# Optimization experiments

Measured on AMD Instinct MI355X. Metric: run time of the kernel, lower is better.

Reference implementation:

```python
import jax, jax.numpy as jnp
import numpy as np

B, R, S, T, D, DK = 256, 196, 200, 50, 512, 100


def setup_inputs() -> dict:
    key = jax.random.key(0)
    ks = jax.random.split(key, 20)
    inp = {
        'ifeature': jax.random.normal(ks[0], (B, R, D), jnp.float32),
        'tfeature_h': jax.random.normal(ks[1], (B, S, D), jnp.float32),
        'gfeature': jax.random.normal(ks[2], (B, S, D), jnp.float32),
        'efeature': jax.random.normal(ks[3], (B, T, D), jnp.float32),
    }
    # learned params (keras 'random_normal' init ~ stddev 0.05, 'zeros' for biases)
    lens = [R, S, S, T]
    for i in range(4):
        inp[f'w_vi{i}'] = 0.05 * jax.random.normal(ks[4 + 4 * i], (D, DK), jnp.float32)
        inp[f'w_vt{i}'] = 0.05 * jax.random.normal(ks[5 + 4 * i], (D, DK), jnp.float32)
        inp[f'w_p{i}'] = 0.05 * jax.random.normal(ks[6 + 4 * i], (2 * DK, 1), jnp.float32)
        inp[f'b{i}'] = jnp.zeros((lens[i],), jnp.float32)
    return inp


def _attend(feats, w_feat, vec, w_vec, w_p, b, vec_first):
    # feats: [B,N,D], vec: [B,D]. Score = concat(tanh parts) @ w_p + b.
    # concat+dense == split w_p into the two halves and add the partial scores.
    k = w_feat.shape[1]
    sf = jnp.tanh(jnp.einsum('bnd,dk->bnk', feats, w_feat))  # [B,N,k]
    sv = jnp.tanh(vec @ w_vec)                               # [B,k]
    if vec_first:
        wv, wf = w_p[:k, 0], w_p[k:, 0]
    else:
        wf, wv = w_p[:k, 0], w_p[k:, 0]
    score = sf @ wf + (sv @ wv)[:, None] + b                 # [B,N]
    p = jax.nn.softmax(score, axis=-1)
    return jnp.einsum('bn,bnd->bd', p, feats)                # [B,D]


def reference(ifeature, tfeature_h, gfeature, efeature,
              w_vi0, w_vt0, w_p0, b0,
              w_vi1, w_vt1, w_p1, b1,
              w_vi2, w_vt2, w_p2, b2,
              w_vi3, w_vt3, w_p3, b3):
    tfeature = jnp.mean(tfeature_h, axis=1)                  # [B,D]
    # block 0: attend over image regions, concat order (image, text)
    Vi = _attend(ifeature, w_vi0, tfeature, w_vt0, w_p0, b0, vec_first=False)
    # block 1: attend over text tokens, concat order (Vi, text)
    Vt = _attend(tfeature_h, w_vt1, Vi, w_vi1, w_p1, b1, vec_first=True)
    # block 2: attend over group feature with query Vi+Vt
    Vg = _attend(gfeature, w_vt2, Vi + Vt, w_vi2, w_p2, b2, vec_first=True)
    # block 3: attend over title feature with query Vi+Vt
    Ve = _attend(efeature, w_vt3, Vi + Vt, w_vi3, w_p3, b3, vec_first=True)
    return Vi + Vt + 0.5 * Vg + 0.5 * Ve
```

## Files before the change

kernel.cpp:

```cpp
#include <hip/hip_runtime.h>

#define DD 512
#define DKk 100
#define NT 7
#define CHUNK 16
#define MAXN 208
#define LDS_STRIDE 520

typedef __attribute__((ext_vector_type(8))) short short8;
typedef __attribute__((ext_vector_type(4))) short short4v;
typedef __attribute__((ext_vector_type(4))) float f32x4;

struct AttendArgs {
  const float* feats[4];
  const float* wfeat[4];
  const float* wf[4];
  const float* bias[4];
  int   N[4];
  float coef[4];
};

__device__ __forceinline__ short f2bf(float x) {
  unsigned u = __builtin_bit_cast(unsigned, x);
  unsigned r = (u + 0x7fffu + ((u >> 16) & 1u)) >> 16;
  return (short)r;
}

__device__ __forceinline__ float fast_tanh(float x) {
  const float e = __expf(2.0f * x);
  return 1.0f - 2.0f / (e + 1.0f);
}

__global__ void wprep_kernel(AttendArgs args, unsigned short* __restrict__ wfrag) {
  const int a = blockIdx.x / NT;
  const int t = blockIdx.x % NT;
  const int tid = threadIdx.x;
  const int lane = tid & 63;
  const int m = lane & 15;
  const int q = lane >> 4;
  const int kg = tid >> 6;
  const int col = t * 16 + m;
  const float* __restrict__ w = args.wfeat[a];
  unsigned short* __restrict__ dst = wfrag + (size_t)((a * NT + t) * 16) * 512;
  #pragma unroll
  for (int i = 0; i < 4; ++i) {
    const int ks = kg * 4 + i;
    short8 v;
    #pragma unroll
    for (int j = 0; j < 8; ++j) {
      const int d = ks * 32 + q * 8 + j;
      v[j] = (col < DKk) ? f2bf(w[d * DKk + col]) : (short)0;
    }
    *reinterpret_cast<short8*>(dst + (size_t)ks * 512 + lane * 8) = v;
  }
}

__global__ __launch_bounds__(512, 2)
void fused_kernel(AttendArgs args, const unsigned short* __restrict__ wfrag,
                  float* __restrict__ out) {
  const int a = blockIdx.x & 3;
  const int b = blockIdx.x >> 2;
  const int tid = threadIdx.x;
  const int lane = tid & 63;
  const int wave = tid >> 6;
  const int m = lane & 15;
  const int q = lane >> 4;
  const int N = args.N[a];
  const float* __restrict__ feats = args.feats[a] + (size_t)b * (size_t)N * DD;
  const float* __restrict__ wfp = args.wf[a];
  const float* __restrict__ bias = args.bias[a];

  __shared__ __align__(16) unsigned short f_lds[2][CHUNK][LDS_STRIDE];
  __shared__ float sc_part[8][MAXN];
  __shared__ float red[512];
  __shared__ float p_lds[MAXN];

  short8 bfrag[16];
  float wfv = 0.f;
  if (wave < NT) {
    const int col = wave * 16 + m;
    wfv = (col < DKk) ? wfp[col] : 0.f;
    const unsigned short* src = wfrag + (size_t)((a * NT + wave) * 16) * 512 + lane * 8;
    #pragma unroll
    for (int ks = 0; ks < 16; ++ks)
      bfrag[ks] = *reinterpret_cast<const short8*>(src + (size_t)ks * 512);
  } else {
    #pragma unroll
    for (int ks = 0; ks < 16; ++ks) bfrag[ks] = short8(0);
  }

  const int nchunks = (N + CHUNK - 1) / CHUNK;

  float4 pf[4];
  #pragma unroll
  for (int it = 0; it < 4; ++it) {
    const int idx = tid + it * 512;
    const int row = idx >> 7;
    const int c4 = idx & 127;
    pf[it] = (row < N)
      ? *reinterpret_cast<const float4*>(feats + (size_t)row * DD + (c4 << 2))
      : make_float4(0.f, 0.f, 0.f, 0.f);
  }

  for (int c = 0; c < nchunks; ++c) {
    const int bufc = c & 1;
    #pragma unroll
    for (int it = 0; it < 4; ++it) {
      const int idx = tid + it * 512;
      const int row = idx >> 7;
      const int c4 = idx & 127;
      short4v pk = { f2bf(pf[it].x), f2bf(pf[it].y), f2bf(pf[it].z), f2bf(pf[it].w) };
      *reinterpret_cast<short4v*>(&f_lds[bufc][row][c4 << 2]) = pk;
    }
    if (c + 1 < nchunks) {
      const int n0n = (c + 1) * CHUNK;
      #pragma unroll
      for (int it = 0; it < 4; ++it) {
        const int idx = tid + it * 512;
        const int row = n0n + (idx >> 7);
        const int c4 = idx & 127;
        pf[it] = (row < N)
          ? *reinterpret_cast<const float4*>(feats + (size_t)row * DD + (c4 << 2))
          : make_float4(0.f, 0.f, 0.f, 0.f);
      }
    }
    __syncthreads();

    if (wave < NT) {
      f32x4 acc = {0.f, 0.f, 0.f, 0.f};
      #pragma unroll
      for (int ks = 0; ks < 16; ++ks) {
        const short8 af = *reinterpret_cast<const short8*>(&f_lds[bufc][m][ks * 32 + q * 8]);
        acc = __builtin_amdgcn_mfma_f32_16x16x32_bf16(af, bfrag[ks], acc, 0, 0, 0);
      }
      float part[4];
      #pragma unroll
      for (int r = 0; r < 4; ++r) part[r] = fast_tanh(acc[r]) * wfv;
      #pragma unroll
      for (int mask = 1; mask <= 8; mask <<= 1) {
        #pragma unroll
        for (int r = 0; r < 4; ++r) part[r] += __shfl_xor(part[r], mask, 64);
      }
      if (m == 0) {
        #pragma unroll
        for (int r = 0; r < 4; ++r) sc_part[wave][c * 16 + q * 4 + r] = part[r];
      }
    } else if (m == 0) {
      #pragma unroll
      for (int r = 0; r < 4; ++r) sc_part[7][c * 16 + q * 4 + r] = 0.f;
    }
  }
  __syncthreads();

  float sval = -1e30f;
  if (tid < N) {
    sval = sc_part[0][tid] + sc_part[1][tid] + sc_part[2][tid] + sc_part[3][tid]
         + sc_part[4][tid] + sc_part[5][tid] + sc_part[6][tid] + sc_part[7][tid]
         + bias[tid];
  }
  red[tid] = sval;
  __syncthreads();
  for (int s = 256; s > 0; s >>= 1) {
    if (tid < s) red[tid] = fmaxf(red[tid], red[tid + s]);
    __syncthreads();
  }
  const float mx = red[0];
  __syncthreads();
  const float e = (tid < N) ? __expf(sval - mx) : 0.f;
  if (tid < MAXN) p_lds[tid] = e;
  red[tid] = e;
  __syncthreads();
  for (int s = 256; s > 0; s >>= 1) {
    if (tid < s) red[tid] += red[tid + s];
    __syncthreads();
  }
  const float scale = args.coef[a] / red[0];

  float acc0 = 0.f, acc1 = 0.f;
  const float* __restrict__ fp = feats + tid;
  const int n4 = N & ~3;
  for (int n = 0; n < n4; n += 4) {
    acc0 += p_lds[n + 0] * fp[(size_t)(n + 0) * DD];
    acc1 += p_lds[n + 1] * fp[(size_t)(n + 1) * DD];
    acc0 += p_lds[n + 2] * fp[(size_t)(n + 2) * DD];
    acc1 += p_lds[n + 3] * fp[(size_t)(n + 3) * DD];
  }
  for (int n = n4; n < N; ++n)
    acc0 += p_lds[n] * fp[(size_t)n * DD];
  atomicAdd(&out[(size_t)b * DD + tid], (acc0 + acc1) * scale);
}

extern "C" void kernel_launch(void* const* d_in, const int* in_sizes, int n_in,
                              void* d_out, int out_size, void* d_ws, size_t ws_size,
                              hipStream_t stream) {
  AttendArgs args;
  args.feats[0] = (const float*)d_in[0];
  args.wfeat[0] = (const float*)d_in[4];
  args.wf[0]    = (const float*)d_in[6];
  args.bias[0]  = (const float*)d_in[7];
  args.N[0] = 196; args.coef[0] = 1.0f;

  args.feats[1] = (const float*)d_in[1];
  args.wfeat[1] = (const float*)d_in[9];
  args.wf[1]    = (const float*)d_in[10] + 100;
  args.bias[1]  = (const float*)d_in[11];
  args.N[1] = 200; args.coef[1] = 1.0f;

  args.feats[2] = (const float*)d_in[2];
  args.wfeat[2] = (const float*)d_in[13];
  args.wf[2]    = (const float*)d_in[14] + 100;
  args.bias[2]  = (const float*)d_in[15];
  args.N[2] = 200; args.coef[2] = 0.5f;

  args.feats[3] = (const float*)d_in[3];
  args.wfeat[3] = (const float*)d_in[17];
  args.wf[3]    = (const float*)d_in[18] + 100;
  args.bias[3]  = (const float*)d_in[19];
  args.N[3] = 50;  args.coef[3] = 0.5f;

  unsigned short* wfrag = (unsigned short*)d_ws;

  hipMemsetAsync(d_out, 0, (size_t)out_size * sizeof(float), stream);
  wprep_kernel<<<dim3(4 * NT), dim3(256), 0, stream>>>(args, wfrag);
  fused_kernel<<<dim3(4 * 256), dim3(512), 0, stream>>>(args, wfrag, (float*)d_out);
}
```

Before: 396.5 us.

## Fuse softmax-weighted pooling into chunk loop using bf16 LDS tiles, drop max pass

The second pass that re-read fp32 features from global memory for the weighted sum is removed. Each chunk's bf16 tile already in LDS is now accumulated with exp(score) weights into per-wave partial sums one iteration behind the score computation, and the partials are reduced at the end. The softmax max-subtraction reduction is dropped and bias is folded into the score partials, which relies on scores staying small enough not to overflow exp. The pooling also now uses bf16-rounded features, which lowers precision, and the weight prep kernel is restructured to stage weights through shared memory.

```diff
diff --git a/kernel.cpp b/kernel.cpp
--- a/kernel.cpp
+++ b/kernel.cpp
@@ -26,32 +26,42 @@
   return (short)r;
 }
 
+__device__ __forceinline__ float bf2f(unsigned short s) {
+  unsigned u = ((unsigned)s) << 16;
+  return __builtin_bit_cast(float, u);
+}
+
 __device__ __forceinline__ float fast_tanh(float x) {
   const float e = __expf(2.0f * x);
   return 1.0f - 2.0f / (e + 1.0f);
 }
 
 __global__ void wprep_kernel(AttendArgs args, unsigned short* __restrict__ wfrag) {
-  const int a = blockIdx.x / NT;
-  const int t = blockIdx.x % NT;
+  const int a   = blockIdx.x >> 2;
+  const int qtr = blockIdx.x & 3;
   const int tid = threadIdx.x;
   const int lane = tid & 63;
   const int m = lane & 15;
   const int q = lane >> 4;
-  const int kg = tid >> 6;
-  const int col = t * 16 + m;
-  const float* __restrict__ w = args.wfeat[a];
-  unsigned short* __restrict__ dst = wfrag + (size_t)((a * NT + t) * 16) * 512;
+  const int sub = tid >> 6;
+  const int ks  = qtr * 4 + sub;
+  __shared__ float wbuf[128 * DKk];
+  const float* __restrict__ w = args.wfeat[a] + (size_t)qtr * 128 * DKk;
   #pragma unroll
-  for (int i = 0; i < 4; ++i) {
-    const int ks = kg * 4 + i;
+  for (int i = 0; i < 50; ++i)
+    wbuf[i * 256 + tid] = w[i * 256 + tid];
+  __syncthreads();
+  #pragma unroll
+  for (int t = 0; t < NT; ++t) {
+    const int col = t * 16 + m;
     short8 v;
     #pragma unroll
     for (int j = 0; j < 8; ++j) {
-      const int d = ks * 32 + q * 8 + j;
-      v[j] = (col < DKk) ? f2bf(w[d * DKk + col]) : (short)0;
-    }
-    *reinterpret_cast<short8*>(dst + (size_t)ks * 512 + lane * 8) = v;
+      const int drel = sub * 32 + q * 8 + j;
+      v[j] = (col < DKk) ? f2bf(wbuf[drel * DKk + col]) : (short)0;
+    }
+    unsigned short* dst = wfrag + (size_t)(((a * NT + t) * 16 + ks) * 512) + lane * 8;
+    *reinterpret_cast<short8*>(dst) = v;
   }
 }
 
@@ -72,8 +82,8 @@
 
   __shared__ __align__(16) unsigned short f_lds[2][CHUNK][LDS_STRIDE];
   __shared__ float sc_part[8][MAXN];
+  __shared__ __align__(16) float partial[8][DD];
   __shared__ float red[512];
-  __shared__ float p_lds[MAXN];
 
   short8 bfrag[16];
   float wfv = 0.f;
@@ -89,7 +99,46 @@
     for (int ks = 0; ks < 16; ++ks) bfrag[ks] = short8(0);
   }
 
+  if (tid < MAXN) sc_part[7][tid] = (tid < N) ? bias[tid] : 0.f;
+  {
+    const f32x4 z = {0.f, 0.f, 0.f, 0.f};
+    *reinterpret_cast<f32x4*>(&partial[wave][lane * 8])     = z;
+    *reinterpret_cast<f32x4*>(&partial[wave][lane * 8 + 4]) = z;
+  }
+
   const int nchunks = (N + CHUNK - 1) / CHUNK;
+
+  auto accum = [&](int pb, int n0) {
+    float* pp = &partial[wave][lane * 8];
+    f32x4 lo = *reinterpret_cast<f32x4*>(pp);
+    f32x4 hi = *reinterpret_cast<f32x4*>(pp + 4);
+    {
+      const int n1 = n0 + wave;
+      const float s1 = sc_part[0][n1] + sc_part[1][n1] + sc_part[2][n1] + sc_part[3][n1]
+                     + sc_part[4][n1] + sc_part[5][n1] + sc_part[6][n1] + sc_part[7][n1];
+      const float e1 = __expf(s1);
+      const short8 f1 = *reinterpret_cast<const short8*>(&f_lds[pb][wave][lane * 8]);
+      #pragma unroll
+      for (int j = 0; j < 4; ++j) {
+        lo[j] = fmaf(e1, bf2f((unsigned short)f1[j]),     lo[j]);
+        hi[j] = fmaf(e1, bf2f((unsigned short)f1[j + 4]), hi[j]);
+      }
+    }
+    {
+      const int n2 = n0 + wave + 8;
+      const float s2 = sc_part[0][n2] + sc_part[1][n2] + sc_part[2][n2] + sc_part[3][n2]
+                     + sc_part[4][n2] + sc_part[5][n2] + sc_part[6][n2] + sc_part[7][n2];
+      const float e2 = __expf(s2);
+      const short8 f2 = *reinterpret_cast<const short8*>(&f_lds[pb][wave + 8][lane * 8]);
+      #pragma unroll
+      for (int j = 0; j < 4; ++j) {
+        lo[j] = fmaf(e2, bf2f((unsigned short)f2[j]),     lo[j]);
+        hi[j] = fmaf(e2, bf2f((unsigned short)f2[j + 4]), hi[j]);
+      }
+    }
+    *reinterpret_cast<f32x4*>(pp)     = lo;
+    *reinterpret_cast<f32x4*>(pp + 4) = hi;
+  };
 
   float4 pf[4];
   #pragma unroll
@@ -145,29 +194,20 @@
         #pragma unroll
         for (int r = 0; r < 4; ++r) sc_part[wave][c * 16 + q * 4 + r] = part[r];
       }
-    } else if (m == 0) {
-      #pragma unroll
-      for (int r = 0; r < 4; ++r) sc_part[7][c * 16 + q * 4 + r] = 0.f;
-    }
-  }
+    }
+    if (c > 0) accum(bufc ^ 1, (c - 1) * CHUNK);
+    __syncthreads();
+  }
+
+  accum((nchunks - 1) & 1, (nchunks - 1) * CHUNK);
   __syncthreads();
 
-  float sval = -1e30f;
+  float e = 0.f;
   if (tid < N) {
-    sval = sc_part[0][tid] + sc_part[1][tid] + sc_part[2][tid] + sc_part[3][tid]
-         + sc_part[4][tid] + sc_part[5][tid] + sc_part[6][tid] + sc_part[7][tid]
-         + bias[tid];
-  }
-  red[tid] = sval;
-  __syncthreads();
-  for (int s = 256; s > 0; s >>= 1) {
-    if (tid < s) red[tid] = fmaxf(red[tid], red[tid + s]);
-    __syncthreads();
-  }
-  const float mx = red[0];
-  __syncthreads();
-  const float e = (tid < N) ? __expf(sval - mx) : 0.f;
-  if (tid < MAXN) p_lds[tid] = e;
+    const float sval = sc_part[0][tid] + sc_part[1][tid] + sc_part[2][tid] + sc_part[3][tid]
+                     + sc_part[4][tid] + sc_part[5][tid] + sc_part[6][tid] + sc_part[7][tid];
+    e = __expf(sval);
+  }
   red[tid] = e;
   __syncthreads();
   for (int s = 256; s > 0; s >>= 1) {
@@ -176,18 +216,9 @@
   }
   const float scale = args.coef[a] / red[0];
 
-  float acc0 = 0.f, acc1 = 0.f;
-  const float* __restrict__ fp = feats + tid;
-  const int n4 = N & ~3;
-  for (int n = 0; n < n4; n += 4) {
-    acc0 += p_lds[n + 0] * fp[(size_t)(n + 0) * DD];
-    acc1 += p_lds[n + 1] * fp[(size_t)(n + 1) * DD];
-    acc0 += p_lds[n + 2] * fp[(size_t)(n + 2) * DD];
-    acc1 += p_lds[n + 3] * fp[(size_t)(n + 3) * DD];
-  }
-  for (int n = n4; n < N; ++n)
-    acc0 += p_lds[n] * fp[(size_t)n * DD];
-  atomicAdd(&out[(size_t)b * DD + tid], (acc0 + acc1) * scale);
+  const float val = partial[0][tid] + partial[1][tid] + partial[2][tid] + partial[3][tid]
+                  + partial[4][tid] + partial[5][tid] + partial[6][tid] + partial[7][tid];
+  atomicAdd(&out[(size_t)b * DD + tid], val * scale);
 }
 
 extern "C" void kernel_launch(void* const* d_in, const int* in_sizes, int n_in,
@@ -221,6 +252,6 @@
   unsigned short* wfrag = (unsigned short*)d_ws;
 
   hipMemsetAsync(d_out, 0, (size_t)out_size * sizeof(float), stream);
-  wprep_kernel<<<dim3(4 * NT), dim3(256), 0, stream>>>(args, wfrag);
+  wprep_kernel<<<dim3(16), dim3(256), 0, stream>>>(args, wfrag);
   fused_kernel<<<dim3(4 * 256), dim3(512), 0, stream>>>(args, wfrag, (float*)d_out);
 }
```

Measured after the change: 366.7 us. 7.5% less time.
